# Performance work log

Measured on AMD Instinct MI355X. Metric: run time of the kernel, lower is better.

Reference implementation:

```python
import jax, jax.numpy as jnp
import numpy as np

N_NODES = 50000
N_EDGES = 600000
F_IN = 128
F_OUT = 128
N_RELS = 8


def setup_inputs() -> dict:
    key = jax.random.key(0)
    k1, k2, k3, k4, k5 = jax.random.split(key, 5)
    X = jax.random.normal(k1, (N_NODES, F_IN), dtype=jnp.float32)
    W = jax.random.normal(k2, (N_RELS, F_OUT, F_IN), dtype=jnp.float32) * (1.0 / np.sqrt(F_IN))
    edge_src = jax.random.randint(k3, (N_EDGES,), 0, N_NODES, dtype=jnp.int32)
    edge_dst = jax.random.randint(k4, (N_EDGES,), 0, N_NODES, dtype=jnp.int32)
    edge_type = jax.random.randint(k5, (N_EDGES,), 0, N_RELS, dtype=jnp.int32)
    return {
        "X": X,
        "W": W,
        "edge_src": edge_src,
        "edge_dst": edge_dst,
        "edge_type": edge_type,
        "num_nodes": N_NODES,
    }


def reference(X, W, edge_src, edge_dst, edge_type, num_nodes):
    # RGCN hetero forward: Y[i, fo] = sum_{edges (j->i) of relation r} W[r, fo, fi] * X[j, fi]
    # Transform all node features by every relation's weight (dense GEMM, high intensity):
    # H[r, n, fo] = sum_fi W[r, fo, fi] * X[n, fi]
    H = jnp.einsum("nf,rof->rno", X, W)  # [R, N, F_out]
    # Gather per-edge messages (relation-specific transformed source feature)
    msgs = H[edge_type, edge_src]  # [E, F_out]
    # Scatter-add messages to destination nodes (the atomic accumulation in the kernel)
    Y = jax.ops.segment_sum(msgs, edge_dst, num_segments=num_nodes)  # [N, F_out]
    return Y
```

## Files before the change

### kernel.cpp

```cpp
#include <hip/hip_runtime.h>

#define F 128
#define RELS 8
#define KMAX 64

typedef __attribute__((ext_vector_type(8))) short short8;
typedef __attribute__((ext_vector_type(4))) float floatx4;

__device__ __forceinline__ unsigned short f2bf(float f) {
    unsigned int u = __float_as_uint(f);
    unsigned int r = (u + 0x7fffu + ((u >> 16) & 1u)) >> 16;
    return (unsigned short)r;
}

__global__ void cvtX_kernel(const float* __restrict__ X, unsigned short* __restrict__ X2, int N) {
    int t = blockIdx.x * blockDim.x + threadIdx.x;
    if (t >= N * (F / 8)) return;
    int n = t >> 4;
    int q = t & 15;
    int fi = q * 8;
    const float* xp = X + (size_t)n * F + fi;
    float4 v0 = *reinterpret_cast<const float4*>(xp);
    float4 v1 = *reinterpret_cast<const float4*>(xp + 4);
    int kc = fi >> 5;
    int ko = fi & 31;
    short8 o;
    o[0] = (short)f2bf(v0.x); o[1] = (short)f2bf(v0.y);
    o[2] = (short)f2bf(v0.z); o[3] = (short)f2bf(v0.w);
    o[4] = (short)f2bf(v1.x); o[5] = (short)f2bf(v1.y);
    o[6] = (short)f2bf(v1.z); o[7] = (short)f2bf(v1.w);
    *reinterpret_cast<short8*>(X2 + ((size_t)(kc * N + n)) * 32 + ko) = o;
}

__global__ void cvtW_kernel(const float* __restrict__ W, unsigned short* __restrict__ W2) {
    int t = blockIdx.x * blockDim.x + threadIdx.x;
    if (t >= RELS * F * (F / 8)) return;
    int r = t >> 11;
    int rem = t & 2047;
    int fo = rem >> 4;
    int qq = rem & 15;
    int fi = qq * 8;
    const float* wp = W + ((size_t)r * F + fo) * F + fi;
    float4 v0 = *reinterpret_cast<const float4*>(wp);
    float4 v1 = *reinterpret_cast<const float4*>(wp + 4);
    int kc = fi >> 5;
    int ko = fi & 31;
    int ct = fo & 7;
    int lr = fo >> 3;
    int q = ct * 16 + lr;
    short8 o;
    o[0] = (short)f2bf(v0.x); o[1] = (short)f2bf(v0.y);
    o[2] = (short)f2bf(v0.z); o[3] = (short)f2bf(v0.w);
    o[4] = (short)f2bf(v1.x); o[5] = (short)f2bf(v1.y);
    o[6] = (short)f2bf(v1.z); o[7] = (short)f2bf(v1.w);
    *reinterpret_cast<short8*>(W2 + ((size_t)((r * 4 + kc) * F + q)) * 32 + ko) = o;
}

__global__ __launch_bounds__(256) void gemm_kernel(const unsigned short* __restrict__ X2,
                                                   const unsigned short* __restrict__ W2,
                                                   unsigned short* __restrict__ H, int N) {
    int lane = threadIdx.x & 63;
    int wave = threadIdx.x >> 6;
    int r = blockIdx.y;
    int row0 = blockIdx.x * 128 + wave * 32;
    int lr = lane & 15;
    int lk = (lane >> 4) * 8;

    short8 a[2][4];
#pragma unroll
    for (int rt = 0; rt < 2; rt++) {
        int row = row0 + rt * 16 + lr;
        if (row > N - 1) row = N - 1;
#pragma unroll
        for (int kc = 0; kc < 4; kc++) {
            a[rt][kc] = *reinterpret_cast<const short8*>(X2 + ((size_t)(kc * N + row)) * 32 + lk);
        }
    }

    floatx4 acc[2][8];
#pragma unroll
    for (int rt = 0; rt < 2; rt++)
#pragma unroll
        for (int ct = 0; ct < 8; ct++)
            acc[rt][ct] = (floatx4){0.f, 0.f, 0.f, 0.f};

#pragma unroll
    for (int ct = 0; ct < 8; ct++) {
        int q = ct * 16 + lr;
#pragma unroll
        for (int kc = 0; kc < 4; kc++) {
            short8 b = *reinterpret_cast<const short8*>(W2 + ((size_t)((r * 4 + kc) * F + q)) * 32 + lk);
            acc[0][ct] = __builtin_amdgcn_mfma_f32_16x16x32_bf16(a[0][kc], b, acc[0][ct], 0, 0, 0);
            acc[1][ct] = __builtin_amdgcn_mfma_f32_16x16x32_bf16(a[1][kc], b, acc[1][ct], 0, 0, 0);
        }
    }

#pragma unroll
    for (int rt = 0; rt < 2; rt++) {
#pragma unroll
        for (int g = 0; g < 4; g++) {
            int row = row0 + rt * 16 + (lane >> 4) * 4 + g;
            short8 o;
#pragma unroll
            for (int ct = 0; ct < 8; ct++) o[ct] = (short)f2bf(acc[rt][ct][g]);
            if (row < N) {
                *reinterpret_cast<short8*>(H + ((size_t)r * N + row) * F + lr * 8) = o;
            }
        }
    }
}

__global__ void fillp_kernel(const int* __restrict__ src, const int* __restrict__ dst,
                             const int* __restrict__ et, int* __restrict__ counts,
                             unsigned int* __restrict__ packed, int E) {
    int t = blockIdx.x * blockDim.x + threadIdx.x;
    if (t >= E) return;
    int d = dst[t];
    int slot = atomicAdd(&counts[d], 1);
    if (slot < KMAX)
        packed[(size_t)d * KMAX + slot] = (unsigned int)src[t] | ((unsigned int)et[t] << 24);
}

__global__ __launch_bounds__(256) void gather_kernel(const unsigned int* __restrict__ H,
                                                     const int* __restrict__ counts,
                                                     const unsigned int* __restrict__ packed,
                                                     float* __restrict__ Y, int N) {
    int node = blockIdx.x * (blockDim.x >> 6) + (threadIdx.x >> 6);
    if (node >= N) return;
    int lane = threadIdx.x & 63;
    int cnt = counts[node];
    if (cnt > KMAX) cnt = KMAX;
    const unsigned int* pk = packed + (size_t)node * KMAX;
    float a0 = 0.f, a1 = 0.f;
    int i = 0;
    for (; i + 4 <= cnt; i += 4) {
        uint4 p = *reinterpret_cast<const uint4*>(pk + i);
        unsigned int v0 = H[((size_t)((p.x >> 24) * N + (p.x & 0xffffffu))) * 64 + lane];
        unsigned int v1 = H[((size_t)((p.y >> 24) * N + (p.y & 0xffffffu))) * 64 + lane];
        unsigned int v2 = H[((size_t)((p.z >> 24) * N + (p.z & 0xffffffu))) * 64 + lane];
        unsigned int v3 = H[((size_t)((p.w >> 24) * N + (p.w & 0xffffffu))) * 64 + lane];
        a0 += __uint_as_float(v0 << 16);
        a1 += __uint_as_float(v0 & 0xffff0000u);
        a0 += __uint_as_float(v1 << 16);
        a1 += __uint_as_float(v1 & 0xffff0000u);
        a0 += __uint_as_float(v2 << 16);
        a1 += __uint_as_float(v2 & 0xffff0000u);
        a0 += __uint_as_float(v3 << 16);
        a1 += __uint_as_float(v3 & 0xffff0000u);
    }
    for (; i < cnt; i++) {
        unsigned int p = pk[i];
        unsigned int v = H[((size_t)((p >> 24) * N + (p & 0xffffffu))) * 64 + lane];
        a0 += __uint_as_float(v << 16);
        a1 += __uint_as_float(v & 0xffff0000u);
    }
    float2 out = make_float2(a0, a1);
    *reinterpret_cast<float2*>(Y + (size_t)node * F + lane * 2) = out;
}

__global__ void fused_fb_kernel(const float* __restrict__ X, const float* __restrict__ W,
                                const int* __restrict__ src, const int* __restrict__ dst,
                                const int* __restrict__ et, float* __restrict__ Y, int E) {
    int lane = threadIdx.x & 63;
    int wid = (blockIdx.x * blockDim.x + threadIdx.x) >> 6;
    int nw = (gridDim.x * blockDim.x) >> 6;
    for (int e = wid; e < E; e += nw) {
        int s = src[e];
        int d = dst[e];
        int r = et[e];
        const float4* xr = reinterpret_cast<const float4*>(X + (size_t)s * F);
#pragma unroll
        for (int h = 0; h < 2; h++) {
            int fo = lane + (h << 6);
            const float4* wr = reinterpret_cast<const float4*>(W + ((size_t)r * F + fo) * F);
            float acc = 0.f;
#pragma unroll
            for (int i = 0; i < 32; i++) {
                float4 x = xr[i];
                float4 w = wr[i];
                acc += x.x * w.x + x.y * w.y + x.z * w.z + x.w * w.w;
            }
            unsafeAtomicAdd(&Y[(size_t)d * F + fo], acc);
        }
    }
}

extern "C" void kernel_launch(void* const* d_in, const int* in_sizes, int n_in,
                              void* d_out, int out_size, void* d_ws, size_t ws_size,
                              hipStream_t stream) {
    const float* X = (const float*)d_in[0];
    const float* W = (const float*)d_in[1];
    const int* src = (const int*)d_in[2];
    const int* dst = (const int*)d_in[3];
    const int* et  = (const int*)d_in[4];
    int N = in_sizes[0] / F;
    int E = in_sizes[2];
    float* Y = (float*)d_out;

    size_t hbytes   = (size_t)RELS * N * F * 2;
    size_t x2bytes  = (size_t)N * F * 2;
    size_t pkbytes  = (size_t)N * KMAX * 4;
    size_t unbytes  = (x2bytes > pkbytes ? x2bytes : pkbytes);
    size_t w2bytes  = (size_t)RELS * F * F * 2;
    size_t cntbytes = ((size_t)N * 4 + 255) & ~255ull;
    size_t need = hbytes + unbytes + w2bytes + cntbytes;

    if (ws_size < need) {
        hipMemsetAsync(d_out, 0, (size_t)N * F * sizeof(float), stream);
        fused_fb_kernel<<<2048, 256, 0, stream>>>(X, W, src, dst, et, Y, E);
        return;
    }

    char* ws = (char*)d_ws;
    unsigned short* H  = (unsigned short*)ws;                 ws += hbytes;
    unsigned short* X2 = (unsigned short*)ws;
    unsigned int* packed = (unsigned int*)X2;                 ws += unbytes;
    unsigned short* W2 = (unsigned short*)ws;                 ws += w2bytes;
    int* counts        = (int*)ws;

    cvtX_kernel<<<(N * (F / 8) + 255) / 256, 256, 0, stream>>>(X, X2, N);
    cvtW_kernel<<<(RELS * F * (F / 8) + 255) / 256, 256, 0, stream>>>(W, W2);
    dim3 g((N + 127) / 128, RELS);
    gemm_kernel<<<g, 256, 0, stream>>>(X2, W2, H, N);

    hipMemsetAsync(counts, 0, (size_t)N * 4, stream);
    fillp_kernel<<<(E + 255) / 256, 256, 0, stream>>>(src, dst, et, counts, packed, E);

    gather_kernel<<<(N + 3) / 4, 256, 0, stream>>>((const unsigned int*)H, counts, packed, Y, N);
}
```

Measured before the change: 208.3 us.

## Aggregate features per relation before transform, fusing gather and GEMM in LDS

Reorders the RGCN computation: each block first sums bf16 source features per relation for a tile of destination nodes into LDS, then multiplies the per-relation sums by the weights with MFMA and writes Y directly. This removes materialising the relation-transformed feature tensor H for all nodes and the wide gather from it, reading the smaller X2 instead. Costs include a large LDS footprint limiting occupancy, a per-edge switch over relation accumulators, and rounding the aggregated sums to bf16 before the GEMM.

Measured after the change: 270.9 us. 30.0% more time.

```diff
diff --git a/kernel.cpp b/kernel.cpp
--- a/kernel.cpp
+++ b/kernel.cpp
@@ -3,6 +3,7 @@
 #define F 128
 #define RELS 8
 #define KMAX 64
+#define NT 32
 
 typedef __attribute__((ext_vector_type(8))) short short8;
 typedef __attribute__((ext_vector_type(4))) float floatx4;
@@ -38,76 +39,19 @@
     int r = t >> 11;
     int rem = t & 2047;
     int fo = rem >> 4;
-    int qq = rem & 15;
-    int fi = qq * 8;
+    int q = rem & 15;
+    int fi = q * 8;
     const float* wp = W + ((size_t)r * F + fo) * F + fi;
     float4 v0 = *reinterpret_cast<const float4*>(wp);
     float4 v1 = *reinterpret_cast<const float4*>(wp + 4);
     int kc = fi >> 5;
     int ko = fi & 31;
-    int ct = fo & 7;
-    int lr = fo >> 3;
-    int q = ct * 16 + lr;
     short8 o;
     o[0] = (short)f2bf(v0.x); o[1] = (short)f2bf(v0.y);
     o[2] = (short)f2bf(v0.z); o[3] = (short)f2bf(v0.w);
     o[4] = (short)f2bf(v1.x); o[5] = (short)f2bf(v1.y);
     o[6] = (short)f2bf(v1.z); o[7] = (short)f2bf(v1.w);
-    *reinterpret_cast<short8*>(W2 + ((size_t)((r * 4 + kc) * F + q)) * 32 + ko) = o;
-}
-
-__global__ __launch_bounds__(256) void gemm_kernel(const unsigned short* __restrict__ X2,
-                                                   const unsigned short* __restrict__ W2,
-                                                   unsigned short* __restrict__ H, int N) {
-    int lane = threadIdx.x & 63;
-    int wave = threadIdx.x >> 6;
-    int r = blockIdx.y;
-    int row0 = blockIdx.x * 128 + wave * 32;
-    int lr = lane & 15;
-    int lk = (lane >> 4) * 8;
-
-    short8 a[2][4];
-#pragma unroll
-    for (int rt = 0; rt < 2; rt++) {
-        int row = row0 + rt * 16 + lr;
-        if (row > N - 1) row = N - 1;
-#pragma unroll
-        for (int kc = 0; kc < 4; kc++) {
-            a[rt][kc] = *reinterpret_cast<const short8*>(X2 + ((size_t)(kc * N + row)) * 32 + lk);
-        }
-    }
-
-    floatx4 acc[2][8];
-#pragma unroll
-    for (int rt = 0; rt < 2; rt++)
-#pragma unroll
-        for (int ct = 0; ct < 8; ct++)
-            acc[rt][ct] = (floatx4){0.f, 0.f, 0.f, 0.f};
-
-#pragma unroll
-    for (int ct = 0; ct < 8; ct++) {
-        int q = ct * 16 + lr;
-#pragma unroll
-        for (int kc = 0; kc < 4; kc++) {
-            short8 b = *reinterpret_cast<const short8*>(W2 + ((size_t)((r * 4 + kc) * F + q)) * 32 + lk);
-            acc[0][ct] = __builtin_amdgcn_mfma_f32_16x16x32_bf16(a[0][kc], b, acc[0][ct], 0, 0, 0);
-            acc[1][ct] = __builtin_amdgcn_mfma_f32_16x16x32_bf16(a[1][kc], b, acc[1][ct], 0, 0, 0);
-        }
-    }
-
-#pragma unroll
-    for (int rt = 0; rt < 2; rt++) {
-#pragma unroll
-        for (int g = 0; g < 4; g++) {
-            int row = row0 + rt * 16 + (lane >> 4) * 4 + g;
-            short8 o;
-#pragma unroll
-            for (int ct = 0; ct < 8; ct++) o[ct] = (short)f2bf(acc[rt][ct][g]);
-            if (row < N) {
-                *reinterpret_cast<short8*>(H + ((size_t)r * N + row) * F + lr * 8) = o;
-            }
-        }
-    }
+    *reinterpret_cast<short8*>(W2 + ((size_t)((r * 4 + kc) * F + fo)) * 32 + ko) = o;
 }
 
 __global__ void fillp_kernel(const int* __restrict__ src, const int* __restrict__ dst,
@@ -121,41 +65,111 @@
         packed[(size_t)d * KMAX + slot] = (unsigned int)src[t] | ((unsigned int)et[t] << 24);
 }
 
-__global__ __launch_bounds__(256) void gather_kernel(const unsigned int* __restrict__ H,
-                                                     const int* __restrict__ counts,
-                                                     const unsigned int* __restrict__ packed,
-                                                     float* __restrict__ Y, int N) {
-    int node = blockIdx.x * (blockDim.x >> 6) + (threadIdx.x >> 6);
-    if (node >= N) return;
+#define LOF(v) __uint_as_float((v) << 16)
+#define HIF(v) __uint_as_float((v) & 0xffff0000u)
+#define ACC(rr, vv)                                                        \
+    {                                                                      \
+        unsigned int _r = (rr);                                            \
+        unsigned int _v = (vv);                                            \
+        switch (_r) {                                                      \
+            case 0: a0x += LOF(_v); a0y += HIF(_v); break;                 \
+            case 1: a1x += LOF(_v); a1y += HIF(_v); break;                 \
+            case 2: a2x += LOF(_v); a2y += HIF(_v); break;                 \
+            case 3: a3x += LOF(_v); a3y += HIF(_v); break;                 \
+            case 4: a4x += LOF(_v); a4y += HIF(_v); break;                 \
+            case 5: a5x += LOF(_v); a5y += HIF(_v); break;                 \
+            case 6: a6x += LOF(_v); a6y += HIF(_v); break;                 \
+            default: a7x += LOF(_v); a7y += HIF(_v); break;                \
+        }                                                                  \
+    }
+
+__global__ __launch_bounds__(256) void fused_kernel(const unsigned int* __restrict__ X2u,
+                                                    const unsigned short* __restrict__ W2,
+                                                    const int* __restrict__ counts,
+                                                    const unsigned int* __restrict__ packed,
+                                                    float* __restrict__ Y, int N) {
+    __shared__ unsigned int Zl[RELS * NT * 64];
     int lane = threadIdx.x & 63;
-    int cnt = counts[node];
-    if (cnt > KMAX) cnt = KMAX;
-    const unsigned int* pk = packed + (size_t)node * KMAX;
-    float a0 = 0.f, a1 = 0.f;
-    int i = 0;
-    for (; i + 4 <= cnt; i += 4) {
-        uint4 p = *reinterpret_cast<const uint4*>(pk + i);
-        unsigned int v0 = H[((size_t)((p.x >> 24) * N + (p.x & 0xffffffu))) * 64 + lane];
-        unsigned int v1 = H[((size_t)((p.y >> 24) * N + (p.y & 0xffffffu))) * 64 + lane];
-        unsigned int v2 = H[((size_t)((p.z >> 24) * N + (p.z & 0xffffffu))) * 64 + lane];
-        unsigned int v3 = H[((size_t)((p.w >> 24) * N + (p.w & 0xffffffu))) * 64 + lane];
-        a0 += __uint_as_float(v0 << 16);
-        a1 += __uint_as_float(v0 & 0xffff0000u);
-        a0 += __uint_as_float(v1 << 16);
-        a1 += __uint_as_float(v1 & 0xffff0000u);
-        a0 += __uint_as_float(v2 << 16);
-        a1 += __uint_as_float(v2 & 0xffff0000u);
-        a0 += __uint_as_float(v3 << 16);
-        a1 += __uint_as_float(v3 & 0xffff0000u);
-    }
-    for (; i < cnt; i++) {
-        unsigned int p = pk[i];
-        unsigned int v = H[((size_t)((p >> 24) * N + (p & 0xffffffu))) * 64 + lane];
-        a0 += __uint_as_float(v << 16);
-        a1 += __uint_as_float(v & 0xffff0000u);
-    }
-    float2 out = make_float2(a0, a1);
-    *reinterpret_cast<float2*>(Y + (size_t)node * F + lane * 2) = out;
+    int wave = threadIdx.x >> 6;
+    int nodebase = blockIdx.x * NT;
+    int lpart = (lane >> 4) * N * 16 + (lane & 15);
+
+#pragma unroll 1
+    for (int i = 0; i < NT / 4; i++) {
+        int nl = wave * (NT / 4) + i;
+        int node = nodebase + nl;
+        float a0x = 0, a0y = 0, a1x = 0, a1y = 0, a2x = 0, a2y = 0, a3x = 0, a3y = 0;
+        float a4x = 0, a4y = 0, a5x = 0, a5y = 0, a6x = 0, a6y = 0, a7x = 0, a7y = 0;
+        if (node < N) {
+            int cnt = counts[node];
+            if (cnt > KMAX) cnt = KMAX;
+            const unsigned int* pk = packed + (size_t)node * KMAX;
+            int e = 0;
+            for (; e + 4 <= cnt; e += 4) {
+                uint4 p = *reinterpret_cast<const uint4*>(pk + e);
+                unsigned int v0 = X2u[lpart + (int)(p.x & 0xffffffu) * 16];
+                unsigned int v1 = X2u[lpart + (int)(p.y & 0xffffffu) * 16];
+                unsigned int v2 = X2u[lpart + (int)(p.z & 0xffffffu) * 16];
+                unsigned int v3 = X2u[lpart + (int)(p.w & 0xffffffu) * 16];
+                ACC(p.x >> 24, v0);
+                ACC(p.y >> 24, v1);
+                ACC(p.z >> 24, v2);
+                ACC(p.w >> 24, v3);
+            }
+            for (; e < cnt; e++) {
+                unsigned int p = pk[e];
+                unsigned int v = X2u[lpart + (int)(p & 0xffffffu) * 16];
+                ACC(p >> 24, v);
+            }
+        }
+        int sl = lane ^ ((nl & 7) << 2);
+        Zl[(0 * NT + nl) * 64 + sl] = (unsigned int)f2bf(a0x) | ((unsigned int)f2bf(a0y) << 16);
+        Zl[(1 * NT + nl) * 64 + sl] = (unsigned int)f2bf(a1x) | ((unsigned int)f2bf(a1y) << 16);
+        Zl[(2 * NT + nl) * 64 + sl] = (unsigned int)f2bf(a2x) | ((unsigned int)f2bf(a2y) << 16);
+        Zl[(3 * NT + nl) * 64 + sl] = (unsigned int)f2bf(a3x) | ((unsigned int)f2bf(a3y) << 16);
+        Zl[(4 * NT + nl) * 64 + sl] = (unsigned int)f2bf(a4x) | ((unsigned int)f2bf(a4y) << 16);
+        Zl[(5 * NT + nl) * 64 + sl] = (unsigned int)f2bf(a5x) | ((unsigned int)f2bf(a5y) << 16);
+        Zl[(6 * NT + nl) * 64 + sl] = (unsigned int)f2bf(a6x) | ((unsigned int)f2bf(a6y) << 16);
+        Zl[(7 * NT + nl) * 64 + sl] = (unsigned int)f2bf(a7x) | ((unsigned int)f2bf(a7y) << 16);
+    }
+    __syncthreads();
+
+    int lr = lane & 15;
+    int lk8 = (lane >> 4) * 8;
+    int nl0 = lr;
+    int nl1 = 16 + lr;
+    floatx4 acc00 = {0, 0, 0, 0}, acc01 = {0, 0, 0, 0}, acc10 = {0, 0, 0, 0}, acc11 = {0, 0, 0, 0};
+#pragma unroll
+    for (int r = 0; r < RELS; r++) {
+#pragma unroll
+        for (int kc = 0; kc < 4; kc++) {
+            int ks = kc * 16 + (lane >> 4) * 4;
+            short8 av0 = *reinterpret_cast<const short8*>(&Zl[(r * NT + nl0) * 64 + (ks ^ ((nl0 & 7) << 2))]);
+            short8 av1 = *reinterpret_cast<const short8*>(&Zl[(r * NT + nl1) * 64 + (ks ^ ((nl1 & 7) << 2))]);
+            short8 b0 = *reinterpret_cast<const short8*>(W2 + ((size_t)((r * 4 + kc) * F + (wave * 2) * 16 + lr)) * 32 + lk8);
+            short8 b1 = *reinterpret_cast<const short8*>(W2 + ((size_t)((r * 4 + kc) * F + (wave * 2 + 1) * 16 + lr)) * 32 + lk8);
+            acc00 = __builtin_amdgcn_mfma_f32_16x16x32_bf16(av0, b0, acc00, 0, 0, 0);
+            acc01 = __builtin_amdgcn_mfma_f32_16x16x32_bf16(av0, b1, acc01, 0, 0, 0);
+            acc10 = __builtin_amdgcn_mfma_f32_16x16x32_bf16(av1, b0, acc10, 0, 0, 0);
+            acc11 = __builtin_amdgcn_mfma_f32_16x16x32_bf16(av1, b1, acc11, 0, 0, 0);
+        }
+    }
+
+    int c0 = (wave * 2) * 16 + lr;
+    int c1 = (wave * 2 + 1) * 16 + lr;
+#pragma unroll
+    for (int g = 0; g < 4; g++) {
+        int row0 = nodebase + (lane >> 4) * 4 + g;
+        if (row0 < N) {
+            Y[(size_t)row0 * F + c0] = acc00[g];
+            Y[(size_t)row0 * F + c1] = acc01[g];
+        }
+        int row1 = nodebase + 16 + (lane >> 4) * 4 + g;
+        if (row1 < N) {
+            Y[(size_t)row1 * F + c0] = acc10[g];
+            Y[(size_t)row1 * F + c1] = acc11[g];
+        }
+    }
 }
 
 __global__ void fused_fb_kernel(const float* __restrict__ X, const float* __restrict__ W,
@@ -197,13 +211,11 @@
     int E = in_sizes[2];
     float* Y = (float*)d_out;
 
-    size_t hbytes   = (size_t)RELS * N * F * 2;
     size_t x2bytes  = (size_t)N * F * 2;
-    size_t pkbytes  = (size_t)N * KMAX * 4;
-    size_t unbytes  = (x2bytes > pkbytes ? x2bytes : pkbytes);
     size_t w2bytes  = (size_t)RELS * F * F * 2;
     size_t cntbytes = ((size_t)N * 4 + 255) & ~255ull;
-    size_t need = hbytes + unbytes + w2bytes + cntbytes;
+    size_t pkbytes  = (size_t)N * KMAX * 4;
+    size_t need = x2bytes + w2bytes + cntbytes + pkbytes;
 
     if (ws_size < need) {
         hipMemsetAsync(d_out, 0, (size_t)N * F * sizeof(float), stream);
@@ -212,19 +224,16 @@
     }
 
     char* ws = (char*)d_ws;
-    unsigned short* H  = (unsigned short*)ws;                 ws += hbytes;
-    unsigned short* X2 = (unsigned short*)ws;
-    unsigned int* packed = (unsigned int*)X2;                 ws += unbytes;
-    unsigned short* W2 = (unsigned short*)ws;                 ws += w2bytes;
-    int* counts        = (int*)ws;
+    unsigned short* X2 = (unsigned short*)ws;  ws += x2bytes;
+    unsigned short* W2 = (unsigned short*)ws;  ws += w2bytes;
+    int* counts        = (int*)ws;             ws += cntbytes;
+    unsigned int* packed = (unsigned int*)ws;
+
+    hipMemsetAsync(counts, 0, (size_t)N * 4, stream);
+    fillp_kernel<<<(E + 255) / 256, 256, 0, stream>>>(src, dst, et, counts, packed, E);
 
     cvtX_kernel<<<(N * (F / 8) + 255) / 256, 256, 0, stream>>>(X, X2, N);
     cvtW_kernel<<<(RELS * F * (F / 8) + 255) / 256, 256, 0, stream>>>(W, W2);
-    dim3 g((N + 127) / 128, RELS);
-    gemm_kernel<<<g, 256, 0, stream>>>(X2, W2, H, N);
-
-    hipMemsetAsync(counts, 0, (size_t)N * 4, stream);
-    fillp_kernel<<<(E + 255) / 256, 256, 0, stream>>>(src, dst, et, counts, packed, E);
-
-    gather_kernel<<<(N + 3) / 4, 256, 0, stream>>>((const unsigned int*)H, counts, packed, Y, N);
-}
+
+    fused_kernel<<<(N + NT - 1) / NT, 256, 0, stream>>>((const unsigned int*)X2, W2, counts, packed, Y, N);
+}
```
